# Optimization experiments

Measured on AMD Instinct MI355X. Metric: run time of the kernel, lower is better.

The kernel has to match this reference:

```python
import jax, jax.numpy as jnp
import numpy as np

D_MODEL = 1024
N_HEADS = 16
HIDDEN = int(D_MODEL * 4 * 2 / 3)  # 2730, matches torch int(d*4*2/3)
EPS = 1e-6


def setup_inputs() -> dict:
    key = jax.random.key(0)
    ks = jax.random.split(key, 8)
    B, T = 4, 2048
    s = 0.02
    return {
        "x": jax.random.normal(ks[0], (B, T, D_MODEL), dtype=jnp.float32),
        "w_attn": jax.random.normal(ks[1], (D_MODEL, 3 * D_MODEL), dtype=jnp.float32) * s,
        "w_proj": jax.random.normal(ks[2], (D_MODEL, D_MODEL), dtype=jnp.float32) * s,
        "w1": jax.random.normal(ks[3], (D_MODEL, HIDDEN), dtype=jnp.float32) * s,
        "w2": jax.random.normal(ks[4], (D_MODEL, HIDDEN), dtype=jnp.float32) * s,
        "w3": jax.random.normal(ks[5], (HIDDEN, D_MODEL), dtype=jnp.float32) * s,
        "g1": jnp.ones((D_MODEL,), dtype=jnp.float32),
        "g2": jnp.ones((D_MODEL,), dtype=jnp.float32),
    }


def rmsnorm(x, g):
    norm = jax.lax.rsqrt(jnp.mean(x * x, axis=-1, keepdims=True) + EPS)
    return x * norm * g


def reference(x, w_attn, w_proj, w1, w2, w3, g1, g2):
    B, T, C = x.shape
    H = N_HEADS
    hd = C // H

    # attention branch
    qkv = rmsnorm(x, g1) @ w_attn                     # [B,T,3C]
    q, k, v = jnp.split(qkv, 3, axis=-1)
    q = q.reshape(B, T, H, hd).transpose(0, 2, 1, 3)  # [B,H,T,hd]
    k = k.reshape(B, T, H, hd).transpose(0, 2, 1, 3)
    v = v.reshape(B, T, H, hd).transpose(0, 2, 1, 3)

    att = jnp.einsum("bhqd,bhkd->bhqk", q, k) / jnp.sqrt(jnp.float32(hd))
    causal = jnp.tril(jnp.ones((T, T), dtype=bool))
    att = jnp.where(causal[None, None], att, jnp.float32(-jnp.inf))
    att = jax.nn.softmax(att, axis=-1)
    y = jnp.einsum("bhqk,bhkd->bhqd", att, v)          # [B,H,T,hd]
    y = y.transpose(0, 2, 1, 3).reshape(B, T, C)
    attn_out = y @ w_proj

    # parallel MLP branch on ln_2(x) (note: applied to x, not x+attn)
    h = rmsnorm(x, g2)
    mlp_out = (jax.nn.silu(h @ w1) * (h @ w2)) @ w3

    # dropout is identity in eval mode
    return x + attn_out + mlp_out
```

## Files before the change

### kernel.cpp

```cpp
#include <hip/hip_runtime.h>

#define TT 2048
#define DM 1024
#define HPAD 2816
#define HID 2730

typedef __attribute__((ext_vector_type(4))) float f32x4;
typedef __attribute__((ext_vector_type(8))) short bf16x8;

static __device__ __forceinline__ float bf2f(short u) {
    union { float f; unsigned int i; } c; c.i = ((unsigned int)(unsigned short)u) << 16; return c.f;
}
static __device__ __forceinline__ short f2bf(float f) {
    union { float f; unsigned int i; } c; c.f = f;
    unsigned int i = c.i;
    unsigned int r = (i + 0x7fffu + ((i >> 16) & 1u)) >> 16;
    return (short)r;
}
static __device__ __forceinline__ short f2bf_trunc(float f) {
    union { float f; unsigned int i; } c; c.f = f;
    return (short)(c.i >> 16);
}

static __device__ __forceinline__ void gload_lds16(const void* g, void* l) {
    __builtin_amdgcn_global_load_lds(
        (const __attribute__((address_space(1))) unsigned int*)g,
        (__attribute__((address_space(3))) unsigned int*)l, 16, 0, 0);
}

__global__ __launch_bounds__(256) void wprep(const float* __restrict__ in, short* __restrict__ out,
                                             int K, int N, int Kpad, int Npad) {
    __shared__ float tile[32][33];
    int kb = blockIdx.x * 32, nb = blockIdx.y * 32;
    int tx = threadIdx.x, ty = threadIdx.y;
    #pragma unroll
    for (int i = 0; i < 32; i += 8) {
        int k = kb + ty + i, n = nb + tx;
        float v = (k < K && n < N) ? in[(size_t)k * N + n] : 0.f;
        tile[tx][ty + i] = v;
    }
    __syncthreads();
    #pragma unroll
    for (int i = 0; i < 32; i += 8) {
        int n = nb + ty + i, k = kb + tx;
        if (n < Npad && k < Kpad) out[(size_t)n * Kpad + k] = f2bf(tile[ty + i][tx]);
    }
}

__global__ __launch_bounds__(256) void rmsnorm2(const float* __restrict__ x,
    const float* __restrict__ g1, const float* __restrict__ g2,
    short* __restrict__ xn1, short* __restrict__ xn2) {
    int row = blockIdx.x;
    const float* xr = x + (size_t)row * DM;
    int t = threadIdx.x;
    float4 v = ((const float4*)xr)[t];
    float ss = v.x*v.x + v.y*v.y + v.z*v.z + v.w*v.w;
    #pragma unroll
    for (int off = 1; off < 64; off <<= 1) ss += __shfl_xor(ss, off);
    __shared__ float red[4];
    if ((t & 63) == 0) red[t >> 6] = ss;
    __syncthreads();
    float tot = red[0] + red[1] + red[2] + red[3];
    float rs = rsqrtf(tot * (1.0f / DM) + 1e-6f);
    float4 G1 = ((const float4*)g1)[t];
    float4 G2 = ((const float4*)g2)[t];
    union { short s[4]; int2 v; } o1, o2;
    o1.s[0] = f2bf(v.x * rs * G1.x); o1.s[1] = f2bf(v.y * rs * G1.y);
    o1.s[2] = f2bf(v.z * rs * G1.z); o1.s[3] = f2bf(v.w * rs * G1.w);
    o2.s[0] = f2bf(v.x * rs * G2.x); o2.s[1] = f2bf(v.y * rs * G2.y);
    o2.s[2] = f2bf(v.z * rs * G2.z); o2.s[3] = f2bf(v.w * rs * G2.w);
    *(int2*)(xn1 + (size_t)row * DM + t * 4) = o1.v;
    *(int2*)(xn2 + (size_t)row * DM + t * 4) = o2.v;
}

template<int EPI>
__global__ __launch_bounds__(256) void gemm_bt(
    const short* __restrict__ A, const short* __restrict__ Bt,
    short* __restrict__ Cb, const float* __restrict__ X, float* __restrict__ Of,
    int M, int N, int K)
{
    __shared__ short As[128 * 64];
    __shared__ short Bs[128 * 64];
    int t = threadIdx.x;
    int wid = t >> 6, l = t & 63;
    int wm = wid >> 1, wn = wid & 1;

    int nwg = gridDim.x, bid = blockIdx.x;
    int wg = (bid & 7) * (nwg >> 3) + (bid >> 3);
    int tiles_n = N >> 7;
    int tm = wg / tiles_n, tn = wg % tiles_n;

    const short* Arow = A + (size_t)(tm * 128) * K;
    const short* Brow = Bt + (size_t)(tn * 128) * K;

    f32x4 acc[4][4];
    #pragma unroll
    for (int m = 0; m < 4; m++)
        #pragma unroll
        for (int n = 0; n < 4; n++) acc[m][n] = (f32x4){0.f, 0.f, 0.f, 0.f};

    for (int kt = 0; kt < K; kt += 64) {
        __syncthreads();
        #pragma unroll
        for (int i = 0; i < 4; i++) {
            int linear = i * 256 + t;
            int row = linear >> 3;
            int slot = linear & 7;
            int srcslot = slot ^ (row & 7);
            gload_lds16(Arow + (size_t)row * K + kt + srcslot * 8, (char*)As + linear * 16);
            gload_lds16(Brow + (size_t)row * K + kt + srcslot * 8, (char*)Bs + linear * 16);
        }
        __syncthreads();
        #pragma unroll
        for (int ks = 0; ks < 2; ks++) {
            bf16x8 af[4], bfr[4];
            #pragma unroll
            for (int m = 0; m < 4; m++) {
                int row = wm * 64 + m * 16 + (l & 15);
                af[m] = *(const bf16x8*)((char*)As + row * 128 + ((ks * 64 + (l >> 4) * 16) ^ ((row & 7) << 4)));
            }
            #pragma unroll
            for (int n = 0; n < 4; n++) {
                int row = wn * 64 + n * 16 + (l & 15);
                bfr[n] = *(const bf16x8*)((char*)Bs + row * 128 + ((ks * 64 + (l >> 4) * 16) ^ ((row & 7) << 4)));
            }
            #pragma unroll
            for (int m = 0; m < 4; m++)
                #pragma unroll
                for (int n = 0; n < 4; n++)
                    acc[m][n] = __builtin_amdgcn_mfma_f32_16x16x32_bf16(af[m], bfr[n], acc[m][n], 0, 0, 0);
        }
    }

    #pragma unroll
    for (int m = 0; m < 4; m++)
        #pragma unroll
        for (int n = 0; n < 4; n++)
            #pragma unroll
            for (int r = 0; r < 4; r++) {
                int row = tm * 128 + wm * 64 + m * 16 + (l >> 4) * 4 + r;
                int col = tn * 128 + wn * 64 + n * 16 + (l & 15);
                size_t idx = (size_t)row * N + col;
                float v = acc[m][n][r];
                if constexpr (EPI == 0) Cb[idx] = f2bf(v);
                else if constexpr (EPI == 1) Of[idx] = X[idx] + v;
                else if constexpr (EPI == 4) Of[idx] += v;
            }
}

__global__ __launch_bounds__(256) void gemm_fuse(
    const short* __restrict__ A1, const short* __restrict__ B1,
    const short* __restrict__ A2, const short* __restrict__ B2,
    const float* __restrict__ X, float* __restrict__ Of)
{
    __shared__ short As[128 * 64];
    __shared__ short Bs[128 * 64];
    int t = threadIdx.x;
    int wid = t >> 6, l = t & 63;
    int wm = wid >> 1, wn = wid & 1;

    int nwg = gridDim.x, bid = blockIdx.x;
    int wg = (bid & 7) * (nwg >> 3) + (bid >> 3);
    int tiles_n = 8;
    int tm = wg / tiles_n, tn = wg % tiles_n;

    f32x4 acc[4][4];
    #pragma unroll
    for (int m = 0; m < 4; m++)
        #pragma unroll
        for (int n = 0; n < 4; n++) acc[m][n] = (f32x4){0.f, 0.f, 0.f, 0.f};

    #pragma unroll 1
    for (int phase = 0; phase < 2; phase++) {
        const short* Arow = phase == 0 ? A1 + (size_t)(tm * 128) * 1024 : A2 + (size_t)(tm * 128) * HPAD;
        const short* Brow = phase == 0 ? B1 + (size_t)(tn * 128) * 1024 : B2 + (size_t)(tn * 128) * HPAD;
        int K = phase == 0 ? 1024 : HPAD;
        for (int kt = 0; kt < K; kt += 64) {
            __syncthreads();
            #pragma unroll
            for (int i = 0; i < 4; i++) {
                int linear = i * 256 + t;
                int row = linear >> 3;
                int slot = linear & 7;
                int srcslot = slot ^ (row & 7);
                gload_lds16(Arow + (size_t)row * K + kt + srcslot * 8, (char*)As + linear * 16);
                gload_lds16(Brow + (size_t)row * K + kt + srcslot * 8, (char*)Bs + linear * 16);
            }
            __syncthreads();
            #pragma unroll
            for (int ks = 0; ks < 2; ks++) {
                bf16x8 af[4], bfr[4];
                #pragma unroll
                for (int m = 0; m < 4; m++) {
                    int row = wm * 64 + m * 16 + (l & 15);
                    af[m] = *(const bf16x8*)((char*)As + row * 128 + ((ks * 64 + (l >> 4) * 16) ^ ((row & 7) << 4)));
                }
                #pragma unroll
                for (int n = 0; n < 4; n++) {
                    int row = wn * 64 + n * 16 + (l & 15);
                    bfr[n] = *(const bf16x8*)((char*)Bs + row * 128 + ((ks * 64 + (l >> 4) * 16) ^ ((row & 7) << 4)));
                }
                #pragma unroll
                for (int m = 0; m < 4; m++)
                    #pragma unroll
                    for (int n = 0; n < 4; n++)
                        acc[m][n] = __builtin_amdgcn_mfma_f32_16x16x32_bf16(af[m], bfr[n], acc[m][n], 0, 0, 0);
            }
        }
    }

    #pragma unroll
    for (int m = 0; m < 4; m++)
        #pragma unroll
        for (int n = 0; n < 4; n++)
            #pragma unroll
            for (int r = 0; r < 4; r++) {
                int row = tm * 128 + wm * 64 + m * 16 + (l >> 4) * 4 + r;
                int col = tn * 128 + wn * 64 + n * 16 + (l & 15);
                size_t idx = (size_t)row * 1024 + col;
                Of[idx] = X[idx] + acc[m][n][r];
            }
}

__global__ __launch_bounds__(512, 2) void gemm_mlp2(
    const short* __restrict__ A, const short* __restrict__ B1t, const short* __restrict__ B2t,
    short* __restrict__ Cb, int M, int N, int K)
{
    __shared__ short As[128 * 64];
    __shared__ short B1s[128 * 64];
    __shared__ short B2s[128 * 64];
    int t = threadIdx.x;
    int wid = t >> 6, l = t & 63;
    int wm = wid >> 2, wn = wid & 3;

    int nwg = gridDim.x, bid = blockIdx.x;
    int wg = (bid & 7) * (nwg >> 3) + (bid >> 3);
    int tiles_n = N >> 7;
    int tm = wg / tiles_n, tn = wg % tiles_n;

    const short* Arow  = A   + (size_t)(tm * 128) * K;
    const short* B1row = B1t + (size_t)(tn * 128) * K;
    const short* B2row = B2t + (size_t)(tn * 128) * K;

    f32x4 acc1[4][2], acc2[4][2];
    #pragma unroll
    for (int m = 0; m < 4; m++)
        #pragma unroll
        for (int n = 0; n < 2; n++) {
            acc1[m][n] = (f32x4){0.f, 0.f, 0.f, 0.f};
            acc2[m][n] = (f32x4){0.f, 0.f, 0.f, 0.f};
        }

    for (int kt = 0; kt < K; kt += 64) {
        __syncthreads();
        #pragma unroll
        for (int i = 0; i < 2; i++) {
            int linear = i * 512 + t;
            int row = linear >> 3;
            int slot = linear & 7;
            int srcslot = slot ^ (row & 7);
            gload_lds16(Arow  + (size_t)row * K + kt + srcslot * 8, (char*)As  + linear * 16);
            gload_lds16(B1row + (size_t)row * K + kt + srcslot * 8, (char*)B1s + linear * 16);
            gload_lds16(B2row + (size_t)row * K + kt + srcslot * 8, (char*)B2s + linear * 16);
        }
        __syncthreads();
        #pragma unroll
        for (int ks = 0; ks < 2; ks++) {
            bf16x8 af[4], b1[2], b2[2];
            #pragma unroll
            for (int m = 0; m < 4; m++) {
                int row = wm * 64 + m * 16 + (l & 15);
                int off = (ks * 64 + (l >> 4) * 16) ^ ((row & 7) << 4);
                af[m] = *(const bf16x8*)((char*)As + row * 128 + off);
            }
            #pragma unroll
            for (int n = 0; n < 2; n++) {
                int row = wn * 32 + n * 16 + (l & 15);
                int off = (ks * 64 + (l >> 4) * 16) ^ ((row & 7) << 4);
                b1[n] = *(const bf16x8*)((char*)B1s + row * 128 + off);
                b2[n] = *(const bf16x8*)((char*)B2s + row * 128 + off);
            }
            #pragma unroll
            for (int m = 0; m < 4; m++)
                #pragma unroll
                for (int n = 0; n < 2; n++) {
                    acc1[m][n] = __builtin_amdgcn_mfma_f32_16x16x32_bf16(af[m], b1[n], acc1[m][n], 0, 0, 0);
                    acc2[m][n] = __builtin_amdgcn_mfma_f32_16x16x32_bf16(af[m], b2[n], acc2[m][n], 0, 0, 0);
                }
        }
    }

    #pragma unroll
    for (int m = 0; m < 4; m++)
        #pragma unroll
        for (int n = 0; n < 2; n++)
            #pragma unroll
            for (int r = 0; r < 4; r++) {
                int row = tm * 128 + wm * 64 + m * 16 + (l >> 4) * 4 + r;
                int col = tn * 128 + wn * 32 + n * 16 + (l & 15);
                float v1 = acc1[m][n][r];
                float v2 = acc2[m][n][r];
                Cb[(size_t)row * N + col] = f2bf(v1 * (1.f / (1.f + __expf(-v1))) * v2);
            }
}

#define PSTR 76
#define SM_C 0.18033688f
__global__ __launch_bounds__(512, 4) void attn(const short* __restrict__ qkv, short* __restrict__ y) {
    __shared__ short Ks[2][64 * 64];
    __shared__ short Vt[2][64 * 64];
    __shared__ short Ps[8][16 * PSTR];
    int bid = blockIdx.x;
    int xcd = bid & 7;
    int idx = bid >> 3;
    int bh  = xcd + 8 * (idx >> 3);
    int pair = idx & 7;
    int b = bh >> 4, h = bh & 15;
    int t = threadIdx.x, wid = t >> 6, l = t & 63;
    const size_t base = (size_t)b * TT * 3072;

    int krow = t >> 3, kslot = t & 7, ksrc = kslot ^ (krow & 7);
    int vrow = t >> 3, vch = t & 7;

    #pragma unroll
    for (int pass = 0; pass < 2; pass++) {
        int qt = pass == 0 ? (15 - pair) : pair;
        int q0 = qt * 128 + wid * 16;

        bf16x8 qf[2];
        #pragma unroll
        for (int s = 0; s < 2; s++) {
            int row = q0 + (l & 15);
            bf16x8 q = *(const bf16x8*)(qkv + base + (size_t)row * 3072 + h * 64 + s * 32 + (l >> 4) * 8);
            #pragma unroll
            for (int i = 0; i < 8; i++) q[i] = f2bf(bf2f(q[i]) * SM_C);
            qf[s] = q;
        }

        f32x4 o[4];
        #pragma unroll
        for (int n = 0; n < 4; n++) o[n] = (f32x4){0.f, 0.f, 0.f, 0.f};
        float ll[4];
        #pragma unroll
        for (int r = 0; r < 4; r++) ll[r] = 0.f;

        int nt = 2 * qt + 2;

        {
            gload_lds16(qkv + base + (size_t)krow * 3072 + 1024 + h * 64 + ksrc * 8,
                        (char*)Ks + t * 16);
            uint4 vv = *(const uint4*)(qkv + base + (size_t)vrow * 3072 + 2048 + h * 64 + vch * 8);
            const short* vs = (const short*)&vv;
            #pragma unroll
            for (int j = 0; j < 8; j++) {
                int d = vch * 8 + j;
                int byte = (d * 128 + vrow * 2) ^ (((j ^ vch) & 7) << 4);
                *(short*)((char*)Vt + byte) = vs[j];
            }
            __syncthreads();
        }

        int cur = 0;
        for (int it = 0; it < nt; ++it) {
            int kb = it << 6;
            bool have_next = (it + 1 < nt);
            uint4 vv;
            if (have_next) {
                int nkb = kb + 64;
                gload_lds16(qkv + base + (size_t)(nkb + krow) * 3072 + 1024 + h * 64 + ksrc * 8,
                            (char*)Ks + (cur ^ 1) * 8192 + t * 16);
                vv = *(const uint4*)(qkv + base + (size_t)(nkb + vrow) * 3072 + 2048 + h * 64 + vch * 8);
            }
            if (kb <= q0 + 15) {
                f32x4 s4[4];
                __builtin_amdgcn_s_setprio(1);
                #pragma unroll
                for (int j = 0; j < 4; j++) {
                    f32x4 z = (f32x4){0.f, 0.f, 0.f, 0.f};
                    #pragma unroll
                    for (int ks = 0; ks < 2; ks++) {
                        int row = j * 16 + (l & 15);
                        bf16x8 kf = *(const bf16x8*)((char*)Ks + cur * 8192 + row * 128 +
                                    ((ks * 64 + (l >> 4) * 16) ^ ((row & 7) << 4)));
                        z = __builtin_amdgcn_mfma_f32_16x16x32_bf16(qf[ks], kf, z, 0, 0, 0);
                    }
                    s4[j] = z;
                }
                __builtin_amdgcn_s_setprio(0);
                bool diag = (kb + 63 > q0);
                #pragma unroll
                for (int j = 0; j < 4; j++)
                    #pragma unroll
                    for (int r = 0; r < 4; r++) {
                        float v = s4[j][r];
                        if (diag) {
                            int qrow = q0 + (l >> 4) * 4 + r;
                            int kcol = kb + j * 16 + (l & 15);
                            if (kcol > qrow) v = -3e38f;
                        }
                        float p = exp2f(v);
                        s4[j][r] = p;
                        ll[r] += p;
                    }

                short* P = &Ps[wid][0];
                #pragma unroll
                for (int j = 0; j < 4; j++)
                    #pragma unroll
                    for (int r = 0; r < 4; r++)
                        P[((l >> 4) * 4 + r) * PSTR + j * 16 + (l & 15)] = f2bf_trunc(s4[j][r]);

                bf16x8 pf[2];
                #pragma unroll
                for (int ks = 0; ks < 2; ks++)
                    pf[ks] = *(const bf16x8*)(P + (l & 15) * PSTR + ks * 32 + (l >> 4) * 8);
                __builtin_amdgcn_s_setprio(1);
                #pragma unroll
                for (int n = 0; n < 4; n++) {
                    #pragma unroll
                    for (int ks = 0; ks < 2; ks++) {
                        int vr = n * 16 + (l & 15);
                        int f = (vr & 7) ^ ((vr >> 3) & 7);
                        bf16x8 vf = *(const bf16x8*)((char*)Vt + cur * 8192 + vr * 128 +
                                    ((ks * 64 + (l >> 4) * 16) ^ (f << 4)));
                        o[n] = __builtin_amdgcn_mfma_f32_16x16x32_bf16(pf[ks], vf, o[n], 0, 0, 0);
                    }
                }
                __builtin_amdgcn_s_setprio(0);
            }
            if (have_next) {
                const short* vs = (const short*)&vv;
                #pragma unroll
                for (int j = 0; j < 8; j++) {
                    int d = vch * 8 + j;
                    int byte = (d * 128 + vrow * 2) ^ (((j ^ vch) & 7) << 4);
                    *(short*)((char*)Vt + (cur ^ 1) * 8192 + byte) = vs[j];
                }
            }
            __syncthreads();
            cur ^= 1;
        }

        #pragma unroll
        for (int r = 0; r < 4; r++) {
            #pragma unroll
            for (int off = 1; off < 16; off <<= 1) ll[r] += __shfl_xor(ll[r], off);
        }
        float inv[4];
        #pragma unroll
        for (int r = 0; r < 4; r++) inv[r] = 1.f / ll[r];
        #pragma unroll
        for (int n = 0; n < 4; n++)
            #pragma unroll
            for (int r = 0; r < 4; r++) {
                int row = q0 + (l >> 4) * 4 + r;
                int col = h * 64 + n * 16 + (l & 15);
                y[(size_t)(b * TT + row) * DM + col] = f2bf(o[n][r] * inv[r]);
            }
    }
}

extern "C" void kernel_launch(void* const* d_in, const int* in_sizes, int n_in,
                              void* d_out, int out_size, void* d_ws, size_t ws_size,
                              hipStream_t stream) {
    (void)in_sizes; (void)n_in; (void)out_size; (void)ws_size;
    const float* x      = (const float*)d_in[0];
    const float* w_attn = (const float*)d_in[1];
    const float* w_proj = (const float*)d_in[2];
    const float* w1     = (const float*)d_in[3];
    const float* w2     = (const float*)d_in[4];
    const float* w3     = (const float*)d_in[5];
    const float* g1     = (const float*)d_in[6];
    const float* g2     = (const float*)d_in[7];
    float* out = (float*)d_out;

    char* ws = (char*)d_ws;
    size_t off = 0;
    auto alloc = [&](size_t bytes) { char* p = ws + off; off += (bytes + 255) & ~(size_t)255; return p; };
    short* wattn_t = (short*)alloc((size_t)3072 * 1024 * 2);
    short* wproj_t = (short*)alloc((size_t)1024 * 1024 * 2);
    short* w1t     = (short*)alloc((size_t)HPAD * 1024 * 2);
    short* w2t     = (short*)alloc((size_t)HPAD * 1024 * 2);
    short* w3t     = (short*)alloc((size_t)1024 * HPAD * 2);
    short* xn1     = (short*)alloc((size_t)8192 * 1024 * 2);
    short* xn2     = (short*)alloc((size_t)8192 * 1024 * 2);
    short* qkvb    = (short*)alloc((size_t)8192 * 3072 * 2);
    short* yb      = (short*)alloc((size_t)8192 * 1024 * 2);
    short* hb      = (short*)alloc((size_t)8192 * HPAD * 2);

    dim3 tb(32, 8);
    wprep<<<dim3(32, 96), tb, 0, stream>>>(w_attn, wattn_t, 1024, 3072, 1024, 3072);
    wprep<<<dim3(32, 32), tb, 0, stream>>>(w_proj, wproj_t, 1024, 1024, 1024, 1024);
    wprep<<<dim3(32, 88), tb, 0, stream>>>(w1, w1t, 1024, HID, 1024, HPAD);
    wprep<<<dim3(32, 88), tb, 0, stream>>>(w2, w2t, 1024, HID, 1024, HPAD);
    wprep<<<dim3(88, 32), tb, 0, stream>>>(w3, w3t, HID, 1024, HPAD, 1024);

    rmsnorm2<<<8192, 256, 0, stream>>>(x, g1, g2, xn1, xn2);

    gemm_bt<0><<<1536, 256, 0, stream>>>(xn1, wattn_t, qkvb, nullptr, nullptr, 8192, 3072, 1024);
    attn<<<512, 512, 0, stream>>>(qkvb, yb);
    gemm_mlp2<<<1408, 512, 0, stream>>>(xn2, w1t, w2t, hb, 8192, HPAD, 1024);
    gemm_fuse<<<512, 256, 0, stream>>>(yb, wproj_t, hb, w3t, x, out);
}
```

Before: 357.8 us.

## Keep attention probabilities in registers via transposed QK^T and lane shuffles

The attention kernel now computes S^T by swapping the MFMA operands, so each lane holds scores for a single query row. It packs exp2 results into bf16 pairs and rearranges them with cross-lane shuffles into the A-operand layout for the PV MFMA. This removes the per-wave LDS staging buffer for P, along with its writes, reads and shared memory footprint. The row-sum becomes one scalar per lane, reduced with two shuffles instead of four per row. In exchange it adds 16 shuffle instructions per tile and changes register pressure.

```diff
diff --git a/kernel.cpp b/kernel.cpp
--- a/kernel.cpp
+++ b/kernel.cpp
@@ -17,9 +17,9 @@
     unsigned int r = (i + 0x7fffu + ((i >> 16) & 1u)) >> 16;
     return (short)r;
 }
-static __device__ __forceinline__ short f2bf_trunc(float f) {
+static __device__ __forceinline__ unsigned int fbits(float f) {
     union { float f; unsigned int i; } c; c.f = f;
-    return (short)(c.i >> 16);
+    return c.i;
 }
 
 static __device__ __forceinline__ void gload_lds16(const void* g, void* l) {
@@ -304,12 +304,10 @@
             }
 }
 
-#define PSTR 76
 #define SM_C 0.18033688f
 __global__ __launch_bounds__(512, 4) void attn(const short* __restrict__ qkv, short* __restrict__ y) {
     __shared__ short Ks[2][64 * 64];
     __shared__ short Vt[2][64 * 64];
-    __shared__ short Ps[8][16 * PSTR];
     int bid = blockIdx.x;
     int xcd = bid & 7;
     int idx = bid >> 3;
@@ -326,6 +324,7 @@
     for (int pass = 0; pass < 2; pass++) {
         int qt = pass == 0 ? (15 - pair) : pair;
         int q0 = qt * 128 + wid * 16;
+        int qrow = q0 + (l & 15);
 
         bf16x8 qf[2];
         #pragma unroll
@@ -340,9 +339,7 @@
         f32x4 o[4];
         #pragma unroll
         for (int n = 0; n < 4; n++) o[n] = (f32x4){0.f, 0.f, 0.f, 0.f};
-        float ll[4];
-        #pragma unroll
-        for (int r = 0; r < 4; r++) ll[r] = 0.f;
+        float ll = 0.f;
 
         int nt = 2 * qt + 2;
 
@@ -372,7 +369,8 @@
                 vv = *(const uint4*)(qkv + base + (size_t)(nkb + vrow) * 3072 + 2048 + h * 64 + vch * 8);
             }
             if (kb <= q0 + 15) {
-                f32x4 s4[4];
+                bool diag = (kb + 63 > q0);
+                unsigned int pk[4][2];
                 __builtin_amdgcn_s_setprio(1);
                 #pragma unroll
                 for (int j = 0; j < 4; j++) {
@@ -382,51 +380,45 @@
                         int row = j * 16 + (l & 15);
                         bf16x8 kf = *(const bf16x8*)((char*)Ks + cur * 8192 + row * 128 +
                                     ((ks * 64 + (l >> 4) * 16) ^ ((row & 7) << 4)));
-                        z = __builtin_amdgcn_mfma_f32_16x16x32_bf16(qf[ks], kf, z, 0, 0, 0);
+                        z = __builtin_amdgcn_mfma_f32_16x16x32_bf16(kf, qf[ks], z, 0, 0, 0);
                     }
-                    s4[j] = z;
-                }
-                __builtin_amdgcn_s_setprio(0);
-                bool diag = (kb + 63 > q0);
-                #pragma unroll
-                for (int j = 0; j < 4; j++)
+                    float p[4];
                     #pragma unroll
                     for (int r = 0; r < 4; r++) {
-                        float v = s4[j][r];
+                        float v = z[r];
                         if (diag) {
-                            int qrow = q0 + (l >> 4) * 4 + r;
-                            int kcol = kb + j * 16 + (l & 15);
+                            int kcol = kb + j * 16 + (l >> 4) * 4 + r;
                             if (kcol > qrow) v = -3e38f;
                         }
-                        float p = exp2f(v);
-                        s4[j][r] = p;
-                        ll[r] += p;
+                        p[r] = exp2f(v);
+                        ll += p[r];
                     }
-
-                short* P = &Ps[wid][0];
-                #pragma unroll
-                for (int j = 0; j < 4; j++)
+                    pk[j][0] = (fbits(p[1]) & 0xffff0000u) | (fbits(p[0]) >> 16);
+                    pk[j][1] = (fbits(p[3]) & 0xffff0000u) | (fbits(p[2]) >> 16);
+                }
+                __builtin_amdgcn_s_setprio(0);
+
+                #pragma unroll
+                for (int ks = 0; ks < 2; ks++) {
+                    union { unsigned int u[4]; bf16x8 v; } pa;
                     #pragma unroll
-                    for (int r = 0; r < 4; r++)
-                        P[((l >> 4) * 4 + r) * PSTR + j * 16 + (l & 15)] = f2bf_trunc(s4[j][r]);
-
-                bf16x8 pf[2];
-                #pragma unroll
-                for (int ks = 0; ks < 2; ks++)
-                    pf[ks] = *(const bf16x8*)(P + (l & 15) * PSTR + ks * 32 + (l >> 4) * 8);
-                __builtin_amdgcn_s_setprio(1);
-                #pragma unroll
-                for (int n = 0; n < 4; n++) {
+                    for (int w = 0; w < 4; w++) {
+                        int src = (((l >> 4) & 1) << 5) | ((w >> 1) << 4) | (l & 15);
+                        unsigned int a = __shfl(pk[2 * ks][w & 1], src);
+                        unsigned int bb = __shfl(pk[2 * ks + 1][w & 1], src);
+                        pa.u[w] = (l >> 5) ? bb : a;
+                    }
+                    __builtin_amdgcn_s_setprio(1);
                     #pragma unroll
-                    for (int ks = 0; ks < 2; ks++) {
+                    for (int n = 0; n < 4; n++) {
                         int vr = n * 16 + (l & 15);
                         int f = (vr & 7) ^ ((vr >> 3) & 7);
                         bf16x8 vf = *(const bf16x8*)((char*)Vt + cur * 8192 + vr * 128 +
                                     ((ks * 64 + (l >> 4) * 16) ^ (f << 4)));
-                        o[n] = __builtin_amdgcn_mfma_f32_16x16x32_bf16(pf[ks], vf, o[n], 0, 0, 0);
+                        o[n] = __builtin_amdgcn_mfma_f32_16x16x32_bf16(pa.v, vf, o[n], 0, 0, 0);
                     }
-                }
-                __builtin_amdgcn_s_setprio(0);
+                    __builtin_amdgcn_s_setprio(0);
+                }
             }
             if (have_next) {
                 const short* vs = (const short*)&vv;
@@ -441,22 +433,19 @@
             cur ^= 1;
         }
 
+        ll += __shfl_xor(ll, 16);
+        ll += __shfl_xor(ll, 32);
+        float inv = 1.f / ll;
         #pragma unroll
         for (int r = 0; r < 4; r++) {
-            #pragma unroll
-            for (int off = 1; off < 16; off <<= 1) ll[r] += __shfl_xor(ll[r], off);
-        }
-        float inv[4];
-        #pragma unroll
-        for (int r = 0; r < 4; r++) inv[r] = 1.f / ll[r];
-        #pragma unroll
-        for (int n = 0; n < 4; n++)
-            #pragma unroll
-            for (int r = 0; r < 4; r++) {
+            float invr = __shfl(inv, (l >> 4) * 4 + r);
+            #pragma unroll
+            for (int n = 0; n < 4; n++) {
                 int row = q0 + (l >> 4) * 4 + r;
                 int col = h * 64 + n * 16 + (l & 15);
-                y[(size_t)(b * TT + row) * DM + col] = f2bf(o[n][r] * inv[r]);
-            }
+                y[(size_t)(b * TT + row) * DM + col] = f2bf(o[n][r] * invr);
+            }
+        }
     }
 }
 
```

Result: faster. 342.8 us (-4.2%).
